# Kernel tuning notes

Measured on AMD Instinct MI355X. Metric: run time of the kernel, lower is better.

## Reference

```python
import jax, jax.numpy as jnp
import numpy as np


def setup_inputs() -> dict:
    key0 = jax.random.key(0)
    ks = jax.random.split(key0, 9)
    B, S, D = 16, 4096, 1024
    inp = {
        "query": jax.random.normal(ks[0], (B, 1, D), dtype=jnp.float32),
        "key": jax.random.normal(ks[1], (B, 1, D), dtype=jnp.float32),
        "value": jax.random.normal(ks[2], (B, 1, D), dtype=jnp.float32),
        "past_key": jax.random.normal(ks[3], (B, S, D), dtype=jnp.float32),
        "past_value": jax.random.normal(ks[4], (B, S, D), dtype=jnp.float32),
        "w_in": jax.random.normal(ks[5], (3 * D, D), dtype=jnp.float32) * 0.02,
        "b_in": jnp.zeros((3 * D,), dtype=jnp.float32),
        "w_out": jax.random.normal(ks[6], (D, D), dtype=jnp.float32) * 0.02,
        "b_out": jnp.zeros((D,), dtype=jnp.float32),
        "nhead": 16,
    }
    return inp


def reference(query, key, value, past_key, past_value, w_in, b_in, w_out, b_out, nhead):
    # concat new step into the raw (pre-projection) KV cache
    comb_key = jnp.concatenate([past_key, key], axis=1)      # (B, S+1, D)
    comb_value = jnp.concatenate([past_value, value], axis=1)  # (B, S+1, D)

    B, _, D = query.shape
    H = nhead
    hd = D // H
    wq, wk, wv = w_in[:D], w_in[D:2 * D], w_in[2 * D:]
    bq, bk, bv = b_in[:D], b_in[D:2 * D], b_in[2 * D:]

    # projections (PyTorch Linear convention: x @ W^T + b)
    q = (query @ wq.T + bq) * (hd ** -0.5)            # (B, 1, D)
    k = comb_key @ wk.T + bk                          # (B, S+1, D)
    v = comb_value @ wv.T + bv                        # (B, S+1, D)

    q = q.reshape(B, 1, H, hd)
    k = k.reshape(B, -1, H, hd)
    v = v.reshape(B, -1, H, hd)

    scores = jnp.einsum("bqhd,bkhd->bhqk", q, k)      # (B, H, 1, S+1)
    attn = jax.nn.softmax(scores, axis=-1)
    ctx = jnp.einsum("bhqk,bkhd->bqhd", attn, v).reshape(B, 1, D)
    out = ctx @ w_out.T + b_out                        # (B, 1, D)
    return out, comb_key, comb_value
```

## Files before the change

### kernel.cpp

```cpp
#include <hip/hip_runtime.h>

#define BB 16
#define SS 4096
#define SC 4097
#define DD 1024
#define HH 16

__device__ __forceinline__ float dot4(const float4 a, const float4 b) {
  return a.x*b.x + a.y*b.y + a.z*b.z + a.w*b.w;
}
__device__ __forceinline__ void fma4(float4& a, const float w, const float4 v) {
  a.x = fmaf(w, v.x, a.x); a.y = fmaf(w, v.y, a.y);
  a.z = fmaf(w, v.z, a.z); a.w = fmaf(w, v.w, a.w);
}
__device__ __forceinline__ void add4(float4& a, const float4 v) {
  a.x += v.x; a.y += v.y; a.z += v.z; a.w += v.w;
}
__device__ __forceinline__ unsigned short f2bf(float x) {
  unsigned int u = __float_as_uint(x);
  u += 0x7fffu + ((u >> 16) & 1u);
  return (unsigned short)(u >> 16);
}

__global__ __launch_bounds__(256, 1) void gemv16(
    const float* __restrict__ X, const float* __restrict__ W,
    const float* __restrict__ bias, const float scale,
    float* __restrict__ Y, const int hsel)
{
  __shared__ float4 xs[4096];
  const int blk = blockIdx.x, t = threadIdx.x;
  const int tp = t >> 4, te = t & 15;
  for (int b = 0; b < BB; ++b) {
    const float* xrow = hsel ? (X + (size_t)(b * 16 + (blk >> 2)) * DD)
                             : (X + (size_t)b * DD);
    xs[b * 256 + tp * 16 + (te ^ (tp & 7))] = ((const float4*)xrow)[t];
  }
  __syncthreads();
  const int dl = tp, part = te;
  const int d = blk * 16 + dl;
  const int sw = part & 7;
  const float4* wrow = (const float4*)(W + (size_t)d * DD) + part * 16;
  float a[BB];
#pragma unroll
  for (int b = 0; b < BB; ++b) a[b] = 0.f;
#pragma unroll
  for (int e4 = 0; e4 < 16; ++e4) {
    const float4 w4 = wrow[e4];
#pragma unroll
    for (int b = 0; b < BB; ++b)
      a[b] += dot4(w4, xs[b * 256 + part * 16 + (e4 ^ sw)]);
  }
#pragma unroll
  for (int b = 0; b < BB; ++b) {
    float v = a[b];
    v += __shfl_xor(v, 1, 64);
    v += __shfl_xor(v, 2, 64);
    v += __shfl_xor(v, 4, 64);
    v += __shfl_xor(v, 8, 64);
    a[b] = v;
  }
  if (part == 0) {
    const float bs = bias[d];
#pragma unroll
    for (int b = 0; b < BB; ++b)
      Y[(size_t)b * DD + d] = (a[b] + bs) * scale;
  }
}

__global__ __launch_bounds__(256, 1) void qw_kernel(
    const float* __restrict__ q, const float* __restrict__ w_in,
    unsigned short* __restrict__ qwbf)
{
  __shared__ float qh[BB * 64];
  const int h = blockIdx.x >> 2, et = blockIdx.x & 3;
  const int t = threadIdx.x;
#pragma unroll
  for (int k = 0; k < 4; ++k) {
    const int i = t + 256 * k;
    qh[i] = q[(i >> 6) * DD + h * 64 + (i & 63)];
  }
  __syncthreads();
  const int e = et * 256 + t;
  const float* wk = w_in + (size_t)(DD + h * 64) * DD + e;
  float a[BB];
#pragma unroll
  for (int b = 0; b < BB; ++b) a[b] = 0.f;
  for (int dh = 0; dh < 64; ++dh) {
    const float wv = wk[(size_t)dh * DD];
#pragma unroll
    for (int b = 0; b < BB; ++b) a[b] = fmaf(qh[b * 64 + dh], wv, a[b]);
  }
#pragma unroll
  for (int b = 0; b < BB; ++b)
    qwbf[(size_t)(b * HH + h) * DD + e] = f2bf(a[b]);
}

template<int CPB>
__global__ __launch_bounds__(256, 1) void attn_main(
    const float* __restrict__ past_key, const float* __restrict__ past_value,
    const float* __restrict__ key_in, const float* __restrict__ value_in,
    const unsigned short* __restrict__ qwbf,
    float* __restrict__ out_ck, float* __restrict__ out_cv,
    float* __restrict__ pvp, float* __restrict__ lp)
{
  constexpr int RPC = SS / CPB;
  constexpr int NG = RPC / 64;
  __shared__ uint2 qws[HH * 256];
  __shared__ float4 Wl[64 * 4];

  const int blk = blockIdx.x;
  const int b = blk / CPB, c = blk % CPB;
  const int t = threadIdx.x, wave = t >> 6, lane = t & 63;

  {
    const uint2* src = (const uint2*)qwbf + (size_t)b * (HH * 256);
#pragma unroll
    for (int i = 0; i < 16; ++i) qws[t + 256 * i] = src[t + 256 * i];
  }

  float4 acc[HH];
#pragma unroll
  for (int h = 0; h < HH; ++h) acc[h] = make_float4(0.f, 0.f, 0.f, 0.f);
  float4 lacc[4];
#pragma unroll
  for (int k = 0; k < 4; ++k) lacc[k] = make_float4(0.f, 0.f, 0.f, 0.f);

  const float4* pk4 = (const float4*)past_key;
  const float4* pv4 = (const float4*)past_value;
  float4* ck4 = (float4*)out_ck;
  float4* cv4 = (float4*)out_cv;

  __syncthreads();

  for (int g = 0; g < NG; ++g) {
    const int gbase = c * RPC + g * 64;
    for (int bt = 0; bt < 4; ++bt) {
      const int r0 = gbase + wave * 16 + bt * 4;
      float p[4][HH];
#pragma unroll
      for (int r = 0; r < 4; ++r)
#pragma unroll
        for (int h = 0; h < HH; ++h) p[r][h] = 0.f;
#pragma unroll
      for (int j = 0; j < 4; ++j) {
        float4 k4[4];
#pragma unroll
        for (int r = 0; r < 4; ++r)
          k4[r] = pk4[(size_t)(b * SS + r0 + r) * 256 + j * 64 + lane];
#pragma unroll
        for (int r = 0; r < 4; ++r)
          ck4[(size_t)(b * SC + r0 + r) * 256 + j * 64 + lane] = k4[r];
#pragma unroll
        for (int h = 0; h < HH; ++h) {
          const uint2 q2 = qws[h * 256 + j * 64 + lane];
          const float f0 = __uint_as_float(q2.x << 16);
          const float f1 = __uint_as_float(q2.x & 0xffff0000u);
          const float f2 = __uint_as_float(q2.y << 16);
          const float f3 = __uint_as_float(q2.y & 0xffff0000u);
#pragma unroll
          for (int r = 0; r < 4; ++r)
            p[r][h] += k4[r].x * f0 + k4[r].y * f1 + k4[r].z * f2 + k4[r].w * f3;
        }
      }
#pragma unroll
      for (int r = 0; r < 4; ++r)
#pragma unroll
        for (int h = 0; h < HH; ++h) {
          float v = p[r][h];
          v += __shfl_xor(v, 32, 64);
          v += __shfl_xor(v, 16, 64);
          v += __shfl_xor(v, 8, 64);
          v += __shfl_xor(v, 4, 64);
          v += __shfl_xor(v, 2, 64);
          v += __shfl_xor(v, 1, 64);
          p[r][h] = v;
        }
#pragma unroll
      for (int h = 0; h < HH; ++h) {
        const float v01 = (lane & 1) ? p[1][h] : p[0][h];
        const float v23 = (lane & 1) ? p[3][h] : p[2][h];
        p[0][h] = (lane & 2) ? v23 : v01;
      }
      if (lane < 4) {
        const int lr = wave * 16 + bt * 4 + lane;
        Wl[lr * 4 + 0] = make_float4(__expf(p[0][0]), __expf(p[0][1]), __expf(p[0][2]), __expf(p[0][3]));
        Wl[lr * 4 + 1] = make_float4(__expf(p[0][4]), __expf(p[0][5]), __expf(p[0][6]), __expf(p[0][7]));
        Wl[lr * 4 + 2] = make_float4(__expf(p[0][8]), __expf(p[0][9]), __expf(p[0][10]), __expf(p[0][11]));
        Wl[lr * 4 + 3] = make_float4(__expf(p[0][12]), __expf(p[0][13]), __expf(p[0][14]), __expf(p[0][15]));
      }
    }
    __syncthreads();
    for (int i = 0; i < 64; ++i) {
      const int s = gbase + i;
      const float4 v4 = pv4[(size_t)(b * SS + s) * 256 + t];
      cv4[(size_t)(b * SC + s) * 256 + t] = v4;
      const float4 w0 = Wl[i * 4 + 0];
      const float4 w1 = Wl[i * 4 + 1];
      const float4 w2 = Wl[i * 4 + 2];
      const float4 w3 = Wl[i * 4 + 3];
      fma4(acc[0], w0.x, v4); fma4(acc[1], w0.y, v4); fma4(acc[2], w0.z, v4); fma4(acc[3], w0.w, v4);
      fma4(acc[4], w1.x, v4); fma4(acc[5], w1.y, v4); fma4(acc[6], w1.z, v4); fma4(acc[7], w1.w, v4);
      fma4(acc[8], w2.x, v4); fma4(acc[9], w2.y, v4); fma4(acc[10], w2.z, v4); fma4(acc[11], w2.w, v4);
      fma4(acc[12], w3.x, v4); fma4(acc[13], w3.y, v4); fma4(acc[14], w3.z, v4); fma4(acc[15], w3.w, v4);
      add4(lacc[0], w0); add4(lacc[1], w1); add4(lacc[2], w2); add4(lacc[3], w3);
    }
    __syncthreads();
  }

  if (c == CPB - 1) {
    if (wave == 0) {
      float p[HH];
#pragma unroll
      for (int h = 0; h < HH; ++h) p[h] = 0.f;
#pragma unroll
      for (int j = 0; j < 4; ++j) {
        const float4 k4 = ((const float4*)key_in)[b * 256 + j * 64 + lane];
        ck4[(size_t)(b * SC + SS) * 256 + j * 64 + lane] = k4;
#pragma unroll
        for (int h = 0; h < HH; ++h) {
          const uint2 q2 = qws[h * 256 + j * 64 + lane];
          const float f0 = __uint_as_float(q2.x << 16);
          const float f1 = __uint_as_float(q2.x & 0xffff0000u);
          const float f2 = __uint_as_float(q2.y << 16);
          const float f3 = __uint_as_float(q2.y & 0xffff0000u);
          p[h] += k4.x * f0 + k4.y * f1 + k4.z * f2 + k4.w * f3;
        }
      }
#pragma unroll
      for (int h = 0; h < HH; ++h) {
        float v = p[h];
        v += __shfl_xor(v, 32, 64);
        v += __shfl_xor(v, 16, 64);
        v += __shfl_xor(v, 8, 64);
        v += __shfl_xor(v, 4, 64);
        v += __shfl_xor(v, 2, 64);
        v += __shfl_xor(v, 1, 64);
        p[h] = v;
      }
      if (lane == 0) {
        Wl[0] = make_float4(__expf(p[0]), __expf(p[1]), __expf(p[2]), __expf(p[3]));
        Wl[1] = make_float4(__expf(p[4]), __expf(p[5]), __expf(p[6]), __expf(p[7]));
        Wl[2] = make_float4(__expf(p[8]), __expf(p[9]), __expf(p[10]), __expf(p[11]));
        Wl[3] = make_float4(__expf(p[12]), __expf(p[13]), __expf(p[14]), __expf(p[15]));
      }
    }
    __syncthreads();
    const float4 v4 = ((const float4*)value_in)[b * 256 + t];
    cv4[(size_t)(b * SC + SS) * 256 + t] = v4;
    const float4 w0 = Wl[0], w1 = Wl[1], w2 = Wl[2], w3 = Wl[3];
    fma4(acc[0], w0.x, v4); fma4(acc[1], w0.y, v4); fma4(acc[2], w0.z, v4); fma4(acc[3], w0.w, v4);
    fma4(acc[4], w1.x, v4); fma4(acc[5], w1.y, v4); fma4(acc[6], w1.z, v4); fma4(acc[7], w1.w, v4);
    fma4(acc[8], w2.x, v4); fma4(acc[9], w2.y, v4); fma4(acc[10], w2.z, v4); fma4(acc[11], w2.w, v4);
    fma4(acc[12], w3.x, v4); fma4(acc[13], w3.y, v4); fma4(acc[14], w3.z, v4); fma4(acc[15], w3.w, v4);
    add4(lacc[0], w0); add4(lacc[1], w1); add4(lacc[2], w2); add4(lacc[3], w3);
  }

  float4* pp = (float4*)pvp + (size_t)blk * (HH * 256);
#pragma unroll
  for (int h = 0; h < HH; ++h) pp[h * 256 + t] = acc[h];
  if (t == 0) {
    float* l = lp + (size_t)blk * HH;
    l[0] = lacc[0].x; l[1] = lacc[0].y; l[2]  = lacc[0].z; l[3]  = lacc[0].w;
    l[4] = lacc[1].x; l[5] = lacc[1].y; l[6]  = lacc[1].z; l[7]  = lacc[1].w;
    l[8] = lacc[2].x; l[9] = lacc[2].y; l[10] = lacc[2].z; l[11] = lacc[2].w;
    l[12] = lacc[3].x; l[13] = lacc[3].y; l[14] = lacc[3].z; l[15] = lacc[3].w;
  }
}

template<int CPB>
__global__ __launch_bounds__(256, 1) void combine_kernel(
    const float* __restrict__ pvp, const float* __restrict__ lp,
    float* __restrict__ pvn)
{
  const int blk = blockIdx.x;
  const int b = blk >> 4, h = blk & 15;
  const int t = threadIdx.x;
  float4 s = make_float4(0.f, 0.f, 0.f, 0.f);
  float l = 0.f;
  for (int c = 0; c < CPB; ++c) {
    const float4* p = (const float4*)pvp + ((size_t)(b * CPB + c) * HH + h) * 256;
    add4(s, p[t]);
    l += lp[(b * CPB + c) * HH + h];
  }
  const float inv = 1.f / l;
  s.x *= inv; s.y *= inv; s.z *= inv; s.w *= inv;
  ((float4*)pvn)[(size_t)blk * 256 + t] = s;
}

extern "C" void kernel_launch(void* const* d_in, const int* in_sizes, int n_in,
                              void* d_out, int out_size, void* d_ws, size_t ws_size,
                              hipStream_t stream)
{
  const float* query      = (const float*)d_in[0];
  const float* key_in     = (const float*)d_in[1];
  const float* value_in   = (const float*)d_in[2];
  const float* past_key   = (const float*)d_in[3];
  const float* past_value = (const float*)d_in[4];
  const float* w_in       = (const float*)d_in[5];
  const float* b_in       = (const float*)d_in[6];
  const float* w_out      = (const float*)d_in[7];
  const float* b_out      = (const float*)d_in[8];

  float* out    = (float*)d_out;
  float* out_ck = out + (size_t)BB * DD;
  float* out_cv = out_ck + (size_t)BB * SC * DD;

  float* ws = (float*)d_ws;
  float* ws_q = ws;
  unsigned short* ws_qwbf = (unsigned short*)(ws_q + BB * DD);
  float* ws_pvn = ws_q + BB * DD + (BB * HH * DD) / 2;
  float* ws_ctx = ws_pvn + (size_t)BB * HH * DD;
  float* ws_pvp = ws_ctx + BB * DD;

  const size_t fixed_f = (size_t)BB * DD + (size_t)(BB * HH * DD) / 2
                       + (size_t)BB * HH * DD + (size_t)BB * DD;
  const size_t need512 = (fixed_f + (size_t)512 * HH * DD + (size_t)512 * HH)
                       * sizeof(float);
  const int big = (ws_size >= need512) ? 1 : 0;

  gemv16<<<64, 256, 0, stream>>>(query, w_in, b_in, 0.125f, ws_q, 0);
  qw_kernel<<<64, 256, 0, stream>>>(ws_q, w_in, ws_qwbf);

  if (big) {
    float* ws_lp = ws_pvp + (size_t)512 * HH * DD;
    attn_main<32><<<512, 256, 0, stream>>>(past_key, past_value, key_in, value_in,
                                           ws_qwbf, out_ck, out_cv, ws_pvp, ws_lp);
    combine_kernel<32><<<256, 256, 0, stream>>>(ws_pvp, ws_lp, ws_pvn);
  } else {
    float* ws_lp = ws_pvp + (size_t)256 * HH * DD;
    attn_main<16><<<256, 256, 0, stream>>>(past_key, past_value, key_in, value_in,
                                           ws_qwbf, out_ck, out_cv, ws_pvp, ws_lp);
    combine_kernel<16><<<256, 256, 0, stream>>>(ws_pvp, ws_lp, ws_pvn);
  }

  gemv16<<<64, 256, 0, stream>>>(ws_pvn, w_in + 2 * DD * DD, b_in + 2 * DD, 1.0f, ws_ctx, 1);
  gemv16<<<64, 256, 0, stream>>>(ws_ctx, w_out, b_out, 1.0f, out, 0);
}
```

Baseline: 1.083 ms.

## Restructure attention kernel into score-then-value phases with 512 threads and nontemporal stores

The attention block now uses 512 threads. It computes exp-scores for all of its rows into shared memory first, then streams the value rows in a second phase with double-buffered float2 loads. The copies of the KV cache into the output use nontemporal stores to avoid polluting the cache. The softmax denominator is summed from shared memory at the end instead of being accumulated per thread. The aim is more memory-level parallelism and fewer barriers, at the cost of a larger shared-memory footprint and a serialized phase structure.

```diff
diff --git a/kernel.cpp b/kernel.cpp
--- a/kernel.cpp
+++ b/kernel.cpp
@@ -9,9 +9,8 @@
 __device__ __forceinline__ float dot4(const float4 a, const float4 b) {
   return a.x*b.x + a.y*b.y + a.z*b.z + a.w*b.w;
 }
-__device__ __forceinline__ void fma4(float4& a, const float w, const float4 v) {
+__device__ __forceinline__ void fma2(float2& a, const float w, const float2 v) {
   a.x = fmaf(w, v.x, a.x); a.y = fmaf(w, v.y, a.y);
-  a.z = fmaf(w, v.z, a.z); a.w = fmaf(w, v.w, a.w);
 }
 __device__ __forceinline__ void add4(float4& a, const float4 v) {
   a.x += v.x; a.y += v.y; a.z += v.z; a.w += v.w;
@@ -20,6 +19,17 @@
   unsigned int u = __float_as_uint(x);
   u += 0x7fffu + ((u >> 16) & 1u);
   return (unsigned short)(u >> 16);
+}
+
+typedef float f32x4 __attribute__((ext_vector_type(4)));
+typedef float f32x2 __attribute__((ext_vector_type(2)));
+__device__ __forceinline__ void nt_store4(float4* p, const float4 v) {
+  f32x4 t = {v.x, v.y, v.z, v.w};
+  __builtin_nontemporal_store(t, (f32x4*)p);
+}
+__device__ __forceinline__ void nt_store2(float2* p, const float2 v) {
+  f32x2 t = {v.x, v.y};
+  __builtin_nontemporal_store(t, (f32x2*)p);
 }
 
 __global__ __launch_bounds__(256, 1) void gemv16(
@@ -96,7 +106,7 @@
 }
 
 template<int CPB>
-__global__ __launch_bounds__(256, 1) void attn_main(
+__global__ __launch_bounds__(512, 4) void attn_main(
     const float* __restrict__ past_key, const float* __restrict__ past_value,
     const float* __restrict__ key_in, const float* __restrict__ value_in,
     const unsigned short* __restrict__ qwbf,
@@ -104,107 +114,128 @@
     float* __restrict__ pvp, float* __restrict__ lp)
 {
   constexpr int RPC = SS / CPB;
-  constexpr int NG = RPC / 64;
+  constexpr int RPW = RPC / 8;
   __shared__ uint2 qws[HH * 256];
-  __shared__ float4 Wl[64 * 4];
+  __shared__ float4 Wl[(RPC + 1) * 4];
 
   const int blk = blockIdx.x;
   const int b = blk / CPB, c = blk % CPB;
   const int t = threadIdx.x, wave = t >> 6, lane = t & 63;
+  const int gbase = c * RPC;
 
   {
     const uint2* src = (const uint2*)qwbf + (size_t)b * (HH * 256);
 #pragma unroll
-    for (int i = 0; i < 16; ++i) qws[t + 256 * i] = src[t + 256 * i];
-  }
-
-  float4 acc[HH];
-#pragma unroll
-  for (int h = 0; h < HH; ++h) acc[h] = make_float4(0.f, 0.f, 0.f, 0.f);
-  float4 lacc[4];
-#pragma unroll
-  for (int k = 0; k < 4; ++k) lacc[k] = make_float4(0.f, 0.f, 0.f, 0.f);
+    for (int i = 0; i < 8; ++i) qws[t + 512 * i] = src[t + 512 * i];
+  }
 
   const float4* pk4 = (const float4*)past_key;
-  const float4* pv4 = (const float4*)past_value;
   float4* ck4 = (float4*)out_ck;
-  float4* cv4 = (float4*)out_cv;
-
   __syncthreads();
 
-  for (int g = 0; g < NG; ++g) {
-    const int gbase = c * RPC + g * 64;
-    for (int bt = 0; bt < 4; ++bt) {
-      const int r0 = gbase + wave * 16 + bt * 4;
-      float p[4][HH];
-#pragma unroll
-      for (int r = 0; r < 4; ++r)
-#pragma unroll
-        for (int h = 0; h < HH; ++h) p[r][h] = 0.f;
-#pragma unroll
-      for (int j = 0; j < 4; ++j) {
-        float4 k4[4];
-#pragma unroll
-        for (int r = 0; r < 4; ++r)
-          k4[r] = pk4[(size_t)(b * SS + r0 + r) * 256 + j * 64 + lane];
-#pragma unroll
-        for (int r = 0; r < 4; ++r)
-          ck4[(size_t)(b * SC + r0 + r) * 256 + j * 64 + lane] = k4[r];
-#pragma unroll
-        for (int h = 0; h < HH; ++h) {
-          const uint2 q2 = qws[h * 256 + j * 64 + lane];
-          const float f0 = __uint_as_float(q2.x << 16);
-          const float f1 = __uint_as_float(q2.x & 0xffff0000u);
-          const float f2 = __uint_as_float(q2.y << 16);
-          const float f3 = __uint_as_float(q2.y & 0xffff0000u);
-#pragma unroll
-          for (int r = 0; r < 4; ++r)
-            p[r][h] += k4[r].x * f0 + k4[r].y * f1 + k4[r].z * f2 + k4[r].w * f3;
-        }
+  for (int bt = 0; bt < RPW / 2; ++bt) {
+    const int lr = wave * RPW + bt * 2;
+    const int r0 = gbase + lr;
+    float4 k0[4], k1[4];
+    const size_t base0 = (size_t)(b * SS + r0) * 256 + lane;
+#pragma unroll
+    for (int j = 0; j < 4; ++j) k0[j] = pk4[base0 + j * 64];
+#pragma unroll
+    for (int j = 0; j < 4; ++j) k1[j] = pk4[base0 + 256 + j * 64];
+    const size_t cb0 = (size_t)(b * SC + r0) * 256 + lane;
+#pragma unroll
+    for (int j = 0; j < 4; ++j) nt_store4(&ck4[cb0 + j * 64], k0[j]);
+#pragma unroll
+    for (int j = 0; j < 4; ++j) nt_store4(&ck4[cb0 + 256 + j * 64], k1[j]);
+
+    float p0[HH], p1[HH];
+#pragma unroll
+    for (int h = 0; h < HH; ++h) { p0[h] = 0.f; p1[h] = 0.f; }
+#pragma unroll
+    for (int j = 0; j < 4; ++j) {
+#pragma unroll
+      for (int h = 0; h < HH; ++h) {
+        const uint2 q2 = qws[h * 256 + j * 64 + lane];
+        const float f0 = __uint_as_float(q2.x << 16);
+        const float f1 = __uint_as_float(q2.x & 0xffff0000u);
+        const float f2 = __uint_as_float(q2.y << 16);
+        const float f3 = __uint_as_float(q2.y & 0xffff0000u);
+        p0[h] += k0[j].x * f0 + k0[j].y * f1 + k0[j].z * f2 + k0[j].w * f3;
+        p1[h] += k1[j].x * f0 + k1[j].y * f1 + k1[j].z * f2 + k1[j].w * f3;
       }
-#pragma unroll
-      for (int r = 0; r < 4; ++r)
-#pragma unroll
-        for (int h = 0; h < HH; ++h) {
-          float v = p[r][h];
-          v += __shfl_xor(v, 32, 64);
-          v += __shfl_xor(v, 16, 64);
-          v += __shfl_xor(v, 8, 64);
-          v += __shfl_xor(v, 4, 64);
-          v += __shfl_xor(v, 2, 64);
-          v += __shfl_xor(v, 1, 64);
-          p[r][h] = v;
-        }
-#pragma unroll
-      for (int h = 0; h < HH; ++h) {
-        const float v01 = (lane & 1) ? p[1][h] : p[0][h];
-        const float v23 = (lane & 1) ? p[3][h] : p[2][h];
-        p[0][h] = (lane & 2) ? v23 : v01;
-      }
-      if (lane < 4) {
-        const int lr = wave * 16 + bt * 4 + lane;
-        Wl[lr * 4 + 0] = make_float4(__expf(p[0][0]), __expf(p[0][1]), __expf(p[0][2]), __expf(p[0][3]));
-        Wl[lr * 4 + 1] = make_float4(__expf(p[0][4]), __expf(p[0][5]), __expf(p[0][6]), __expf(p[0][7]));
-        Wl[lr * 4 + 2] = make_float4(__expf(p[0][8]), __expf(p[0][9]), __expf(p[0][10]), __expf(p[0][11]));
-        Wl[lr * 4 + 3] = make_float4(__expf(p[0][12]), __expf(p[0][13]), __expf(p[0][14]), __expf(p[0][15]));
-      }
-    }
-    __syncthreads();
-    for (int i = 0; i < 64; ++i) {
-      const int s = gbase + i;
-      const float4 v4 = pv4[(size_t)(b * SS + s) * 256 + t];
-      cv4[(size_t)(b * SC + s) * 256 + t] = v4;
-      const float4 w0 = Wl[i * 4 + 0];
-      const float4 w1 = Wl[i * 4 + 1];
-      const float4 w2 = Wl[i * 4 + 2];
-      const float4 w3 = Wl[i * 4 + 3];
-      fma4(acc[0], w0.x, v4); fma4(acc[1], w0.y, v4); fma4(acc[2], w0.z, v4); fma4(acc[3], w0.w, v4);
-      fma4(acc[4], w1.x, v4); fma4(acc[5], w1.y, v4); fma4(acc[6], w1.z, v4); fma4(acc[7], w1.w, v4);
-      fma4(acc[8], w2.x, v4); fma4(acc[9], w2.y, v4); fma4(acc[10], w2.z, v4); fma4(acc[11], w2.w, v4);
-      fma4(acc[12], w3.x, v4); fma4(acc[13], w3.y, v4); fma4(acc[14], w3.z, v4); fma4(acc[15], w3.w, v4);
-      add4(lacc[0], w0); add4(lacc[1], w1); add4(lacc[2], w2); add4(lacc[3], w3);
-    }
-    __syncthreads();
+    }
+#pragma unroll
+    for (int h = 0; h < HH; ++h) {
+      float v0 = p0[h], v1 = p1[h];
+      v0 += __shfl_xor(v0, 32, 64); v1 += __shfl_xor(v1, 32, 64);
+      v0 += __shfl_xor(v0, 16, 64); v1 += __shfl_xor(v1, 16, 64);
+      v0 += __shfl_xor(v0, 8, 64);  v1 += __shfl_xor(v1, 8, 64);
+      v0 += __shfl_xor(v0, 4, 64);  v1 += __shfl_xor(v1, 4, 64);
+      v0 += __shfl_xor(v0, 2, 64);  v1 += __shfl_xor(v1, 2, 64);
+      v0 += __shfl_xor(v0, 1, 64);  v1 += __shfl_xor(v1, 1, 64);
+      p0[h] = v0; p1[h] = v1;
+    }
+    float e[HH];
+#pragma unroll
+    for (int h = 0; h < HH; ++h) e[h] = __expf((lane & 1) ? p1[h] : p0[h]);
+    if (lane < 2) {
+      const int wr = lr + lane;
+      Wl[wr * 4 + 0] = make_float4(e[0],  e[1],  e[2],  e[3]);
+      Wl[wr * 4 + 1] = make_float4(e[4],  e[5],  e[6],  e[7]);
+      Wl[wr * 4 + 2] = make_float4(e[8],  e[9],  e[10], e[11]);
+      Wl[wr * 4 + 3] = make_float4(e[12], e[13], e[14], e[15]);
+    }
+  }
+  __syncthreads();
+
+  const float2* pv2 = (const float2*)past_value;
+  float2* cv2 = (float2*)out_cv;
+  float2 acc[HH];
+#pragma unroll
+  for (int h = 0; h < HH; ++h) acc[h] = make_float2(0.f, 0.f);
+
+  const size_t vbase = (size_t)(b * SS + gbase) * 512 + t;
+  const size_t cvb   = (size_t)(b * SC + gbase) * 512 + t;
+  float2 va[4], vb[4];
+#pragma unroll
+  for (int r = 0; r < 4; ++r) va[r] = pv2[vbase + (size_t)r * 512];
+  for (int i0 = 0; i0 < RPC; i0 += 8) {
+#pragma unroll
+    for (int r = 0; r < 4; ++r) vb[r] = pv2[vbase + (size_t)(i0 + 4 + r) * 512];
+#pragma unroll
+    for (int r = 0; r < 4; ++r) {
+      const int i = i0 + r;
+      nt_store2(&cv2[cvb + (size_t)i * 512], va[r]);
+      const float4 w0 = Wl[i * 4 + 0], w1 = Wl[i * 4 + 1];
+      const float4 w2 = Wl[i * 4 + 2], w3 = Wl[i * 4 + 3];
+      fma2(acc[0],  w0.x, va[r]); fma2(acc[1],  w0.y, va[r]);
+      fma2(acc[2],  w0.z, va[r]); fma2(acc[3],  w0.w, va[r]);
+      fma2(acc[4],  w1.x, va[r]); fma2(acc[5],  w1.y, va[r]);
+      fma2(acc[6],  w1.z, va[r]); fma2(acc[7],  w1.w, va[r]);
+      fma2(acc[8],  w2.x, va[r]); fma2(acc[9],  w2.y, va[r]);
+      fma2(acc[10], w2.z, va[r]); fma2(acc[11], w2.w, va[r]);
+      fma2(acc[12], w3.x, va[r]); fma2(acc[13], w3.y, va[r]);
+      fma2(acc[14], w3.z, va[r]); fma2(acc[15], w3.w, va[r]);
+    }
+    if (i0 + 8 < RPC) {
+#pragma unroll
+      for (int r = 0; r < 4; ++r) va[r] = pv2[vbase + (size_t)(i0 + 8 + r) * 512];
+    }
+#pragma unroll
+    for (int r = 0; r < 4; ++r) {
+      const int i = i0 + 4 + r;
+      nt_store2(&cv2[cvb + (size_t)i * 512], vb[r]);
+      const float4 w0 = Wl[i * 4 + 0], w1 = Wl[i * 4 + 1];
+      const float4 w2 = Wl[i * 4 + 2], w3 = Wl[i * 4 + 3];
+      fma2(acc[0],  w0.x, vb[r]); fma2(acc[1],  w0.y, vb[r]);
+      fma2(acc[2],  w0.z, vb[r]); fma2(acc[3],  w0.w, vb[r]);
+      fma2(acc[4],  w1.x, vb[r]); fma2(acc[5],  w1.y, vb[r]);
+      fma2(acc[6],  w1.z, vb[r]); fma2(acc[7],  w1.w, vb[r]);
+      fma2(acc[8],  w2.x, vb[r]); fma2(acc[9],  w2.y, vb[r]);
+      fma2(acc[10], w2.z, vb[r]); fma2(acc[11], w2.w, vb[r]);
+      fma2(acc[12], w3.x, vb[r]); fma2(acc[13], w3.y, vb[r]);
+      fma2(acc[14], w3.z, vb[r]); fma2(acc[15], w3.w, vb[r]);
+    }
   }
 
   if (c == CPB - 1) {
@@ -215,7 +246,7 @@
 #pragma unroll
       for (int j = 0; j < 4; ++j) {
         const float4 k4 = ((const float4*)key_in)[b * 256 + j * 64 + lane];
-        ck4[(size_t)(b * SC + SS) * 256 + j * 64 + lane] = k4;
+        nt_store4(&ck4[(size_t)(b * SC + SS) * 256 + j * 64 + lane], k4);
 #pragma unroll
         for (int h = 0; h < HH; ++h) {
           const uint2 q2 = qws[h * 256 + j * 64 + lane];
@@ -238,33 +269,41 @@
         p[h] = v;
       }
       if (lane == 0) {
-        Wl[0] = make_float4(__expf(p[0]), __expf(p[1]), __expf(p[2]), __expf(p[3]));
-        Wl[1] = make_float4(__expf(p[4]), __expf(p[5]), __expf(p[6]), __expf(p[7]));
-        Wl[2] = make_float4(__expf(p[8]), __expf(p[9]), __expf(p[10]), __expf(p[11]));
-        Wl[3] = make_float4(__expf(p[12]), __expf(p[13]), __expf(p[14]), __expf(p[15]));
+        Wl[RPC * 4 + 0] = make_float4(__expf(p[0]),  __expf(p[1]),  __expf(p[2]),  __expf(p[3]));
+        Wl[RPC * 4 + 1] = make_float4(__expf(p[4]),  __expf(p[5]),  __expf(p[6]),  __expf(p[7]));
+        Wl[RPC * 4 + 2] = make_float4(__expf(p[8]),  __expf(p[9]),  __expf(p[10]), __expf(p[11]));
+        Wl[RPC * 4 + 3] = make_float4(__expf(p[12]), __expf(p[13]), __expf(p[14]), __expf(p[15]));
       }
     }
     __syncthreads();
-    const float4 v4 = ((const float4*)value_in)[b * 256 + t];
-    cv4[(size_t)(b * SC + SS) * 256 + t] = v4;
-    const float4 w0 = Wl[0], w1 = Wl[1], w2 = Wl[2], w3 = Wl[3];
-    fma4(acc[0], w0.x, v4); fma4(acc[1], w0.y, v4); fma4(acc[2], w0.z, v4); fma4(acc[3], w0.w, v4);
-    fma4(acc[4], w1.x, v4); fma4(acc[5], w1.y, v4); fma4(acc[6], w1.z, v4); fma4(acc[7], w1.w, v4);
-    fma4(acc[8], w2.x, v4); fma4(acc[9], w2.y, v4); fma4(acc[10], w2.z, v4); fma4(acc[11], w2.w, v4);
-    fma4(acc[12], w3.x, v4); fma4(acc[13], w3.y, v4); fma4(acc[14], w3.z, v4); fma4(acc[15], w3.w, v4);
-    add4(lacc[0], w0); add4(lacc[1], w1); add4(lacc[2], w2); add4(lacc[3], w3);
-  }
-
-  float4* pp = (float4*)pvp + (size_t)blk * (HH * 256);
-#pragma unroll
-  for (int h = 0; h < HH; ++h) pp[h * 256 + t] = acc[h];
-  if (t == 0) {
-    float* l = lp + (size_t)blk * HH;
-    l[0] = lacc[0].x; l[1] = lacc[0].y; l[2]  = lacc[0].z; l[3]  = lacc[0].w;
-    l[4] = lacc[1].x; l[5] = lacc[1].y; l[6]  = lacc[1].z; l[7]  = lacc[1].w;
-    l[8] = lacc[2].x; l[9] = lacc[2].y; l[10] = lacc[2].z; l[11] = lacc[2].w;
-    l[12] = lacc[3].x; l[13] = lacc[3].y; l[14] = lacc[3].z; l[15] = lacc[3].w;
-  }
+    const float2 v2 = ((const float2*)value_in)[b * 512 + t];
+    nt_store2(&cv2[(size_t)(b * SC + SS) * 512 + t], v2);
+    const float4 w0 = Wl[RPC * 4 + 0], w1 = Wl[RPC * 4 + 1];
+    const float4 w2 = Wl[RPC * 4 + 2], w3 = Wl[RPC * 4 + 3];
+    fma2(acc[0],  w0.x, v2); fma2(acc[1],  w0.y, v2);
+    fma2(acc[2],  w0.z, v2); fma2(acc[3],  w0.w, v2);
+    fma2(acc[4],  w1.x, v2); fma2(acc[5],  w1.y, v2);
+    fma2(acc[6],  w1.z, v2); fma2(acc[7],  w1.w, v2);
+    fma2(acc[8],  w2.x, v2); fma2(acc[9],  w2.y, v2);
+    fma2(acc[10], w2.z, v2); fma2(acc[11], w2.w, v2);
+    fma2(acc[12], w3.x, v2); fma2(acc[13], w3.y, v2);
+    fma2(acc[14], w3.z, v2); fma2(acc[15], w3.w, v2);
+  }
+
+  if (wave == 0) {
+    const int h = lane & 15, q = lane >> 4;
+    float s = 0.f;
+    const float* Wf = (const float*)Wl;
+    const int nrows = RPC + ((c == CPB - 1) ? 1 : 0);
+    for (int i = q; i < nrows; i += 4) s += Wf[i * 16 + h];
+    s += __shfl_xor(s, 16, 64);
+    s += __shfl_xor(s, 32, 64);
+    if (lane < 16) lp[(size_t)blk * HH + lane] = s;
+  }
+
+  float2* pp = (float2*)pvp + (size_t)blk * (HH * 512);
+#pragma unroll
+  for (int h = 0; h < HH; ++h) pp[h * 512 + t] = acc[h];
 }
 
 template<int CPB>
@@ -323,12 +362,12 @@
 
   if (big) {
     float* ws_lp = ws_pvp + (size_t)512 * HH * DD;
-    attn_main<32><<<512, 256, 0, stream>>>(past_key, past_value, key_in, value_in,
+    attn_main<32><<<512, 512, 0, stream>>>(past_key, past_value, key_in, value_in,
                                            ws_qwbf, out_ck, out_cv, ws_pvp, ws_lp);
     combine_kernel<32><<<256, 256, 0, stream>>>(ws_pvp, ws_lp, ws_pvn);
   } else {
     float* ws_lp = ws_pvp + (size_t)256 * HH * DD;
-    attn_main<16><<<256, 256, 0, stream>>>(past_key, past_value, key_in, value_in,
+    attn_main<16><<<256, 512, 0, stream>>>(past_key, past_value, key_in, value_in,
                                            ws_qwbf, out_ck, out_cv, ws_pvp, ws_lp);
     combine_kernel<16><<<256, 256, 0, stream>>>(ws_pvp, ws_lp, ws_pvn);
   }
```

Result: slower. 1.191 ms (+10.0%).
